# Optimization experiments

Measured on AMD Instinct MI355X. Metric: run time of the kernel, lower is better.

Reference implementation:

```python
import jax, jax.numpy as jnp
import numpy as np

B, HW, D, CL, K, V, NL, H = 16, 4096, 512, 768, 512, 512, 32, 8
EPS = 1e-5

def conv1d(x, w, b):
    # 1x1 Conv1d: x (B, Cin, L), w (Cout, Cin), b (Cout,)
    return jnp.einsum('oi,bil->bol', w, x) + b[:, None]

def inorm(x):
    # InstanceNorm1d (affine=False, biased var) over the length dim per channel
    m = jnp.mean(x, axis=-1, keepdims=True)
    v = jnp.var(x, axis=-1, keepdims=True)
    return (x - m) / jnp.sqrt(v + EPS)

def _forward(x, l, l_mask, w_vis, b_vis, w_langp, b_langp, w_q, b_q, w_k, b_k,
             w_v, b_v, w_lv, b_lv, w_W, b_W, w_langW, b_langW,
             w_mm, b_mm, w_langmm, b_langmm):
    xt = x.transpose(0, 2, 1)                       # (B, D, HW)
    mask = l_mask.transpose(0, 2, 1)                # (B, 1, NL)
    vis = jax.nn.gelu(conv1d(xt, w_vis, b_vis), approximate=False)      # (B, D, HW)
    lang = jax.nn.gelu(conv1d(l, w_langp, b_langp), approximate=False)  # (B, CL, NL)

    q = inorm(conv1d(xt, w_q, b_q)).transpose(0, 2, 1)   # (B, HW, K)
    k = conv1d(l, w_k, b_k) * mask                       # (B, K, NL)
    v = conv1d(l, w_v, b_v) * mask                       # (B, V, NL)
    lv = inorm(conv1d(xt, w_lv, b_lv))                   # (B, CL, HW)

    q = q.reshape(B, HW, H, K // H).transpose(0, 2, 1, 3)   # (B, H, HW, dk)
    k = k.reshape(B, H, K // H, NL)
    v = v.reshape(B, H, V // H, NL)
    lv = lv.reshape(B, H, CL // H, HW)

    # note: scale uses FULL key_channels (as in the torch code), mask bias added once
    sim = jnp.einsum('bhqd,bhdn->bhqn', q, k) * (K ** -0.5)
    sim = sim + (10000.0 * mask[:, :, None, :] - 10000.0)    # (B, H, HW, NL)

    att = jax.nn.softmax(sim, axis=-1)                         # image -> lang
    latt = jax.nn.softmax(sim.transpose(0, 1, 3, 2), axis=-1)  # lang -> image

    lang_out = jnp.einsum('bhnq,bhcq->bhcn', latt, lv).reshape(B, CL, NL) * mask
    lang_out = inorm(conv1d(lang_out, w_langW, b_langW))       # (B, CL, NL)

    out = jnp.einsum('bhqn,bhdn->bqhd', att, v).reshape(B, HW, V)
    vis_out = inorm(conv1d(out.transpose(0, 2, 1), w_W, b_W))  # (B, V, HW)

    mm = jax.nn.gelu(conv1d(vis * vis_out, w_mm, b_mm), approximate=False)
    lang_mm = jax.nn.gelu(conv1d(lang * lang_out, w_langmm, b_langmm), approximate=False)
    return mm.transpose(0, 2, 1), lang_mm.transpose(0, 2, 1)   # (B,HW,V), (B,NL,CL)

def setup_inputs():
    key = jax.random.key(0)
    ks = jax.random.split(key, 24)
    inp = {}
    inp['x'] = jax.random.normal(ks[0], (B, HW, D), jnp.float32)
    inp['l'] = jax.random.normal(ks[1], (B, CL, NL), jnp.float32)
    lengths = jax.random.randint(ks[2], (B, 1), 5, NL + 1)
    inp['l_mask'] = (jnp.arange(NL)[None, :] < lengths).astype(jnp.float32)[:, :, None]
    specs = [('vis', D, D), ('langp', CL, CL), ('q', K, D), ('k', K, CL),
             ('v', V, CL), ('lv', CL, D), ('W', V, V), ('langW', CL, CL),
             ('mm', V, V), ('langmm', CL, CL)]
    for i, (n, o, ci) in enumerate(specs):
        inp['w_' + n] = jax.random.normal(ks[3 + 2 * i], (o, ci), jnp.float32) / float(np.sqrt(ci))
        inp['b_' + n] = jax.random.normal(ks[4 + 2 * i], (o,), jnp.float32) * 0.01
    return inp

def reference(x, l, l_mask, w_vis, b_vis, w_langp, b_langp, w_q, b_q, w_k, b_k,
              w_v, b_v, w_lv, b_lv, w_W, b_W, w_langW, b_langW,
              w_mm, b_mm, w_langmm, b_langmm):
    return _forward(x, l, l_mask, w_vis, b_vis, w_langp, b_langp, w_q, b_q, w_k, b_k,
                    w_v, b_v, w_lv, b_lv, w_W, b_W, w_langW, b_langW,
                    w_mm, b_mm, w_langmm, b_langmm)
```

## Files before the change

kernel.cpp:

```cpp
#include <hip/hip_runtime.h>
#include <cstdint>
#include <cstddef>


typedef __bf16 bf16x8 __attribute__((ext_vector_type(8)));
typedef float f32x4 __attribute__((ext_vector_type(4)));
typedef unsigned short ushort8 __attribute__((ext_vector_type(8)));

__device__ __forceinline__ float bf2f(unsigned short u) {
  union { unsigned int i; float f; } c; c.i = ((unsigned int)u) << 16; return c.f;
}
__device__ __forceinline__ unsigned short f2bf(float f) {
  union { float f; unsigned int i; } c; c.f = f;
  unsigned int r = c.i + 0x7FFFu + ((c.i >> 16) & 1u);
  return (unsigned short)(r >> 16);
}
__device__ __forceinline__ float gelu_f(float x) {
  return 0.5f * x * (1.f + erff(x * 0.70710678118654752f));
}
__device__ __forceinline__ void gload16(const void* g, void* l) {
  __builtin_amdgcn_global_load_lds(
      (__attribute__((address_space(1))) unsigned int*)g,
      (__attribute__((address_space(3))) unsigned int*)l, 16, 0, 0);
}

constexpr size_t OFF_SRQ  = 0;
constexpr size_t OFF_SRLV = OFF_SRQ  + (size_t)16*512*2*4;
constexpr size_t OFF_SRW  = OFF_SRLV + (size_t)16*768*2*4;
constexpr size_t OFF_LACC = OFF_SRW  + (size_t)16*512*2*4;
constexpr size_t SZ_ZERO  = OFF_LACC + (size_t)16*768*32*4;
constexpr size_t OFF_STQ  = SZ_ZERO;
constexpr size_t OFF_STLV = OFF_STQ  + (size_t)16*512*2*4;
constexpr size_t OFF_STW  = OFF_STLV + (size_t)16*768*2*4;
constexpr size_t OFF_KBUF = OFF_STW  + (size_t)16*512*2*4;
constexpr size_t OFF_VBUF = OFF_KBUF + (size_t)16*512*32*4;
constexpr size_t OFF_LANG = OFF_VBUF + (size_t)16*512*32*4;
constexpr size_t OFF_LMX  = OFF_LANG + (size_t)16*768*32*4;
constexpr size_t OFF_LSM  = OFF_LMX  + (size_t)128*32*4;
constexpr size_t OFF_LNORM= OFF_LSM  + (size_t)128*32*4;
constexpr size_t OFF_P2   = OFF_LNORM+ (size_t)16*768*32*4;
constexpr size_t OFF_PMX  = OFF_P2   + (size_t)16*768*32*4;
constexpr size_t OFF_PSM  = OFF_PMX  + (size_t)32*128*32*4;
constexpr size_t OFF_WB   = OFF_PSM  + (size_t)32*128*32*4;
constexpr size_t OFF_Q    = OFF_WB   + (size_t)1441792*2;
constexpr size_t OFF_LV   = OFF_Q    + (size_t)65536*512*2;
constexpr size_t OFF_SIMB = OFF_LV   + (size_t)65536*768*2;

__global__ __launch_bounds__(256) void cvt_bf16(const float* __restrict__ src,
                                                unsigned short* __restrict__ dst, int n8)
{
  int i = blockIdx.x * 256 + threadIdx.x;
  if (i >= n8) return;
  const f32x4* s = (const f32x4*)(src + (size_t)i * 8);
  f32x4 a = s[0], b = s[1];
  ushort8 o;
#pragma unroll
  for (int j = 0; j < 4; ++j) { o[j] = f2bf(a[j]); o[j + 4] = f2bf(b[j]); }
  *(ushort8*)(dst + (size_t)i * 8) = o;
}

template<bool GELU, bool STATS, bool OUTF32>
__global__ __launch_bounds__(256) void gemm_bt(
    const unsigned short* __restrict__ A, const unsigned short* __restrict__ Wb,
    const float* __restrict__ bias, void* __restrict__ Yout,
    float* __restrict__ statsraw, int N, int Kd)
{
  __shared__ __align__(16) unsigned short As[128 * 64];
  __shared__ __align__(16) unsigned short Bs[128 * 64];
  const int t = threadIdx.x;
  const int wave = t >> 6, lane = t & 63;
  const int ln = lane & 15, quad = lane >> 4;
  const int m0 = blockIdx.x * 128, n0 = blockIdx.y * 128;
  const int wm = (wave >> 1) * 64, wn = (wave & 1) * 64;
  const f32x4 fzero = {0.f, 0.f, 0.f, 0.f};
  f32x4 acc[4][4];
#pragma unroll
  for (int i = 0; i < 4; ++i)
#pragma unroll
    for (int j = 0; j < 4; ++j) acc[i][j] = fzero;
  const int lrow = lane >> 3;
  const int lch  = lane & 7;

  for (int k0 = 0; k0 < Kd; k0 += 64) {
#pragma unroll
    for (int it = 0; it < 4; ++it) {
      int g = wave * 4 + it;
      int row = g * 8 + lrow;
      gload16(A  + (size_t)(m0 + row) * Kd + k0 + lch * 8, &As[g * 512]);
      gload16(Wb + (size_t)(n0 + row) * Kd + k0 + lch * 8, &Bs[g * 512]);
    }
    __syncthreads();
#pragma unroll
    for (int kk = 0; kk < 64; kk += 32) {
      int c = (kk >> 3) + quad;
      bf16x8 af[4], bfr[4];
#pragma unroll
      for (int i = 0; i < 4; ++i)
        af[i] = *(const bf16x8*)&As[(wm + i * 16 + ln) * 64 + c * 8];
#pragma unroll
      for (int j = 0; j < 4; ++j)
        bfr[j] = *(const bf16x8*)&Bs[(wn + j * 16 + ln) * 64 + c * 8];
#pragma unroll
      for (int i = 0; i < 4; ++i)
#pragma unroll
        for (int j = 0; j < 4; ++j)
          acc[i][j] = __builtin_amdgcn_mfma_f32_16x16x32_bf16(af[i], bfr[j], acc[i][j], 0, 0, 0);
    }
    __syncthreads();
  }
  float bb[4];
#pragma unroll
  for (int j = 0; j < 4; ++j) bb[j] = bias[n0 + wn + j * 16 + ln];
#pragma unroll
  for (int i = 0; i < 4; ++i)
#pragma unroll
    for (int j = 0; j < 4; ++j)
#pragma unroll
      for (int r = 0; r < 4; ++r) {
        float v = acc[i][j][r] + bb[j];
        if (GELU) v = gelu_f(v);
        acc[i][j][r] = v;
        size_t row = (size_t)(m0 + wm + i * 16 + quad * 4 + r);
        size_t idx = row * N + (n0 + wn + j * 16 + ln);
        if (OUTF32) ((float*)Yout)[idx] = v;
        else ((unsigned short*)Yout)[idx] = f2bf(v);
      }
  if (STATS) {
    float* cs = (float*)As;
    cs[t] = 0.f;
    __syncthreads();
#pragma unroll
    for (int j = 0; j < 4; ++j) {
      float s = 0.f, s2 = 0.f;
#pragma unroll
      for (int i = 0; i < 4; ++i)
#pragma unroll
        for (int r = 0; r < 4; ++r) { float v = acc[i][j][r]; s += v; s2 += v * v; }
      int cl = wn + j * 16 + ln;
      atomicAdd(&cs[cl], s);
      atomicAdd(&cs[128 + cl], s2);
    }
    __syncthreads();
    int bIdx = m0 >> 12;
    if (t < 128) atomicAdd(&statsraw[((size_t)bIdx * N + n0 + t) * 2], cs[t]);
    else atomicAdd(&statsraw[((size_t)bIdx * N + n0 + (t - 128)) * 2 + 1], cs[t]);
  }
}

__global__ void finalize_stats(const float* __restrict__ raw, float* __restrict__ st,
                               int n, float invc) {
  int i = blockIdx.x * 256 + threadIdx.x;
  if (i >= n) return;
  float s = raw[2 * i], s2 = raw[2 * i + 1];
  float m = s * invc;
  float v = fmaxf(s2 * invc - m * m, 0.f);
  st[2 * i] = m;
  st[2 * i + 1] = rsqrtf(v + 1e-5f);
}

template<int EPI>
__global__ __launch_bounds__(256) void sconv(
    const float* __restrict__ l, const float* __restrict__ w,
    const float* __restrict__ bias, const float* __restrict__ lmask,
    float* __restrict__ out, int O, int Cin)
{
  int b = blockIdx.x, og = blockIdx.y;
  int ol = threadIdx.x >> 5, n = threadIdx.x & 31;
  int o = og * 8 + ol;
  const float* lb = l + (size_t)b * Cin * 32 + n;
  const float* wr = w + (size_t)o * Cin;
  float s = 0.f;
#pragma unroll 4
  for (int i = 0; i < Cin; ++i) s += wr[i] * lb[(size_t)i * 32];
  s += bias[o];
  if (EPI == 0) s *= lmask[b * 32 + n];
  else s = gelu_f(s);
  out[((size_t)b * O + o) * 32 + n] = s;
}

__global__ __launch_bounds__(256) void simattv_kernel(
    const unsigned short* __restrict__ qraw, const float* __restrict__ stq,
    const float* __restrict__ kbuf, const float* __restrict__ vbuf,
    const float* __restrict__ lmask,
    unsigned short* __restrict__ simb, unsigned short* __restrict__ outb,
    float* __restrict__ pmx, float* __restrict__ psm)
{
  __shared__ __align__(16) float qs[128][68];
  __shared__ __align__(16) float ks[64][36];
  __shared__ __align__(16) float vs[64][36];
  __shared__ __align__(16) float ss[128][36];
  __shared__ float sm[64], sr[64], mb[32];
  __shared__ float gm[8][32], gs[8][32];
  int qc = blockIdx.x, q0 = qc * 128, h = blockIdx.y, b = blockIdx.z;
  int bh = b * 8 + h;
  int t = threadIdx.x;
  if (t < 64) {
    sm[t] = stq[(b * 512 + h * 64 + t) * 2];
    sr[t] = stq[(b * 512 + h * 64 + t) * 2 + 1];
  } else if (t < 96) {
    mb[t - 64] = 10000.f * (lmask[b * 32 + (t - 64)] - 1.f);
  }
  for (int e = t; e < 2048; e += 256) {
    int d = e >> 5, n = e & 31;
    ks[d][n] = kbuf[((size_t)b * 512 + h * 64 + d) * 32 + n];
    vs[d][n] = vbuf[((size_t)b * 512 + h * 64 + d) * 32 + n];
  }
  __syncthreads();
  const float scale = 0.04419417382415922f;
  for (int e = t; e < 8192; e += 256) {
    int ql = e >> 6, d = e & 63;
    float v = bf2f(qraw[((size_t)(b * 4096) + q0 + ql) * 512 + h * 64 + d]);
    qs[ql][d] = (v - sm[d]) * sr[d] * scale;
  }
  __syncthreads();
  int ql = t >> 1, half = t & 1, nb = half * 16;
  float acc[16];
#pragma unroll
  for (int i = 0; i < 16; ++i) acc[i] = 0.f;
  for (int d = 0; d < 64; ++d) {
    float qv = qs[ql][d];
    const f32x4* kp = (const f32x4*)&ks[d][nb];
#pragma unroll
    for (int u = 0; u < 4; ++u) {
      f32x4 kv = kp[u];
      acc[u * 4 + 0] += qv * kv[0]; acc[u * 4 + 1] += qv * kv[1];
      acc[u * 4 + 2] += qv * kv[2]; acc[u * 4 + 3] += qv * kv[3];
    }
  }
  unsigned short* sg = simb + (((size_t)bh) * 4096 + q0 + ql) * 32 + nb;
#pragma unroll
  for (int i = 0; i < 16; ++i) {
    float v = acc[i] + mb[nb + i];
    ss[ql][nb + i] = v;
    sg[i] = f2bf(v);
  }
  __syncthreads();
  {
    int n2 = t & 31, rg = t >> 5;
    float pm = -1e30f;
#pragma unroll
    for (int r = 0; r < 16; ++r) pm = fmaxf(pm, ss[rg * 16 + r][n2]);
    float psv = 0.f;
#pragma unroll
    for (int r = 0; r < 16; ++r) psv += __expf(ss[rg * 16 + r][n2] - pm);
    gm[rg][n2] = pm; gs[rg][n2] = psv;
  }
  __syncthreads();
  if (t < 32) {
    float M = gm[0][t], S = gs[0][t];
#pragma unroll
    for (int g = 1; g < 8; ++g) {
      float m2 = gm[g][t], s2 = gs[g][t];
      if (m2 > M) { S = S * __expf(M - m2) + s2; M = m2; }
      else S += s2 * __expf(m2 - M);
    }
    pmx[((size_t)qc * 128 + bh) * 32 + t] = M;
    psm[((size_t)qc * 128 + bh) * 32 + t] = S;
  }
  __syncthreads();
  float xv[16];
  float mx = -1e30f;
#pragma unroll
  for (int i = 0; i < 16; ++i) { xv[i] = ss[ql][nb + i]; mx = fmaxf(mx, xv[i]); }
  mx = fmaxf(mx, __shfl_xor(mx, 1));
  float s = 0.f;
#pragma unroll
  for (int i = 0; i < 16; ++i) { xv[i] = __expf(xv[i] - mx); s += xv[i]; }
  s += __shfl_xor(s, 1);
  float inv = 1.f / s;
#pragma unroll
  for (int i = 0; i < 16; ++i) ss[ql][nb + i] = xv[i] * inv;
  __syncthreads();
  float pr[32];
#pragma unroll
  for (int i = 0; i < 8; ++i) ((f32x4*)pr)[i] = ((const f32x4*)&ss[ql][0])[i];
  unsigned short* op = outb + ((size_t)b * 4096 + q0 + ql) * 512 + h * 64 + half * 32;
#pragma unroll
  for (int d = 0; d < 32; ++d) {
    const float* vr = &vs[half * 32 + d][0];
    float a = 0.f;
#pragma unroll
    for (int n4 = 0; n4 < 8; ++n4) {
      f32x4 v4 = *(const f32x4*)&vr[n4 * 4];
      a += pr[n4 * 4 + 0] * v4[0] + pr[n4 * 4 + 1] * v4[1] +
           pr[n4 * 4 + 2] * v4[2] + pr[n4 * 4 + 3] * v4[3];
    }
    op[d] = f2bf(a);
  }
}

__global__ __launch_bounds__(256) void latt_merge(const float* __restrict__ pmx,
                                                  const float* __restrict__ psm,
                                                  float* __restrict__ lmx,
                                                  float* __restrict__ lsm)
{
  int i = blockIdx.x * 256 + threadIdx.x;
  int bh = i >> 5, n = i & 31;
  float M = -1e30f, S = 0.f;
#pragma unroll 4
  for (int c = 0; c < 32; ++c) {
    float m2 = pmx[((size_t)c * 128 + bh) * 32 + n];
    float s2 = psm[((size_t)c * 128 + bh) * 32 + n];
    if (m2 > M) { S = S * __expf(M - m2) + s2; M = m2; }
    else S += s2 * __expf(m2 - M);
  }
  lmx[bh * 32 + n] = M;
  lsm[bh * 32 + n] = S;
}

__global__ __launch_bounds__(256) void langout_acc_kernel(
    const unsigned short* __restrict__ simb, const float* __restrict__ lmx,
    const float* __restrict__ lsm, const unsigned short* __restrict__ lvraw,
    const float* __restrict__ stlv, float* __restrict__ lacc)
{
  __shared__ __align__(16) float pt[64][32];
  __shared__ __align__(16) float lvt[64][96];
  __shared__ float cm[96], cr[96], lm[32], li[32];
  int bh = blockIdx.x, b = bh >> 3, h = bh & 7;
  int qs0 = blockIdx.y * 512;
  int t = threadIdx.x;
  if (t < 96) { cm[t] = stlv[(b * 768 + h * 96 + t) * 2]; cr[t] = stlv[(b * 768 + h * 96 + t) * 2 + 1]; }
  else if (t >= 128 && t < 160) {
    int n = t - 128;
    lm[n] = lmx[bh * 32 + n];
    li[n] = 1.f / lsm[bh * 32 + n];
  }
  __syncthreads();
  int n = t & 31, cg = t >> 5;
  float acc[12];
#pragma unroll
  for (int r = 0; r < 12; ++r) acc[r] = 0.f;
  for (int c0 = 0; c0 < 512; c0 += 64) {
    if (c0) __syncthreads();
#pragma unroll
    for (int i = 0; i < 8; ++i) {
      int e = t + 256 * i;
      int ql = e >> 5, nn = e & 31;
      float x = bf2f(simb[((size_t)bh * 4096 + qs0 + c0 + ql) * 32 + nn]);
      pt[ql][nn] = __expf(x - lm[nn]) * li[nn];
    }
#pragma unroll
    for (int i = 0; i < 24; ++i) {
      int e = t + 256 * i;
      int ql = e / 96, cc = e % 96;
      float v = bf2f(lvraw[((size_t)(b * 4096) + qs0 + c0 + ql) * 768 + h * 96 + cc]);
      lvt[ql][cc] = (v - cm[cc]) * cr[cc];
    }
    __syncthreads();
    for (int q = 0; q < 64; ++q) {
      float pv = pt[q][n];
      const f32x4* lp = (const f32x4*)&lvt[q][cg * 12];
      f32x4 a0 = lp[0], a1 = lp[1], a2 = lp[2];
      acc[0] += pv * a0[0]; acc[1] += pv * a0[1]; acc[2]  += pv * a0[2]; acc[3]  += pv * a0[3];
      acc[4] += pv * a1[0]; acc[5] += pv * a1[1]; acc[6]  += pv * a1[2]; acc[7]  += pv * a1[3];
      acc[8] += pv * a2[0]; acc[9] += pv * a2[1]; acc[10] += pv * a2[2]; acc[11] += pv * a2[3];
    }
  }
#pragma unroll
  for (int r = 0; r < 12; ++r)
    atomicAdd(&lacc[((size_t)b * 768 + h * 96 + cg * 12 + r) * 32 + n], acc[r]);
}

__global__ __launch_bounds__(256) void prod_kernel(
    const unsigned short* __restrict__ visb, const unsigned short* __restrict__ wraw,
    const float* __restrict__ stw, unsigned short* __restrict__ P)
{
  size_t idx = ((size_t)blockIdx.x * 256 + threadIdx.x) * 8;
  int b = (int)(idx >> 21);
  int c = (int)(idx & 511);
  ushort8 vv = *(const ushort8*)&visb[idx];
  ushort8 wv = *(const ushort8*)&wraw[idx];
  ushort8 pv;
#pragma unroll
  for (int i = 0; i < 8; ++i) {
    float mean = stw[(b * 512 + c + i) * 2], rs = stw[(b * 512 + c + i) * 2 + 1];
    pv[i] = f2bf(bf2f(vv[i]) * ((bf2f(wv[i]) - mean) * rs));
  }
  *(ushort8*)&P[idx] = pv;
}

__global__ __launch_bounds__(256) void langW_kernel(
    const float* __restrict__ lacc, const float* __restrict__ w,
    const float* __restrict__ bias, const float* __restrict__ lmask,
    float* __restrict__ lnorm)
{
  int b = blockIdx.x, og = blockIdx.y;
  int ol = threadIdx.x >> 5, n = threadIdx.x & 31;
  int o = og * 8 + ol;
  const float* ab = lacc + (size_t)b * 768 * 32 + n;
  const float* wr = w + (size_t)o * 768;
  float s = 0.f;
#pragma unroll 4
  for (int i = 0; i < 768; ++i) s += wr[i] * ab[(size_t)i * 32];
  float y = s * lmask[b * 32 + n] + bias[o];
  float m = y;
#pragma unroll
  for (int off = 16; off >= 1; off >>= 1) m += __shfl_xor(m, off);
  m *= (1.f / 32.f);
  float d = y - m;
  float vv = d * d;
#pragma unroll
  for (int off = 16; off >= 1; off >>= 1) vv += __shfl_xor(vv, off);
  vv *= (1.f / 32.f);
  lnorm[((size_t)b * 768 + o) * 32 + n] = d * rsqrtf(vv + 1e-5f);
}

__global__ __launch_bounds__(256) void p2_kernel(const float* __restrict__ a,
                                                 const float* __restrict__ b,
                                                 float* __restrict__ o, int n) {
  int i = blockIdx.x * 256 + threadIdx.x;
  if (i < n) o[i] = a[i] * b[i];
}

__global__ __launch_bounds__(256) void langmm_kernel(
    const float* __restrict__ p2, const float* __restrict__ w,
    const float* __restrict__ bias, float* __restrict__ out1)
{
  int b = blockIdx.x, og = blockIdx.y;
  int ol = threadIdx.x >> 5, n = threadIdx.x & 31;
  int o = og * 8 + ol;
  const float* pb = p2 + (size_t)b * 768 * 32 + n;
  const float* wr = w + (size_t)o * 768;
  float s = 0.f;
#pragma unroll 4
  for (int i = 0; i < 768; ++i) s += wr[i] * pb[(size_t)i * 32];
  s = gelu_f(s + bias[o]);
  __shared__ float tile[8][32];
  tile[ol][n] = s;
  __syncthreads();
  int nn = threadIdx.x >> 3, cl = threadIdx.x & 7;
  out1[((size_t)b * 32 + nn) * 768 + og * 8 + cl] = tile[cl][nn];
}

extern "C" void kernel_launch(void* const* d_in, const int* in_sizes, int n_in,
                              void* d_out, int out_size, void* d_ws, size_t ws_size,
                              hipStream_t stream)
{
  (void)in_sizes; (void)n_in; (void)out_size; (void)ws_size;
  const float* x       = (const float*)d_in[0];
  const float* l       = (const float*)d_in[1];
  const float* lmask   = (const float*)d_in[2];
  const float* w_vis   = (const float*)d_in[3];
  const float* b_vis   = (const float*)d_in[4];
  const float* w_langp = (const float*)d_in[5];
  const float* b_langp = (const float*)d_in[6];
  const float* w_q     = (const float*)d_in[7];
  const float* b_q     = (const float*)d_in[8];
  const float* w_k     = (const float*)d_in[9];
  const float* b_k     = (const float*)d_in[10];
  const float* w_v     = (const float*)d_in[11];
  const float* b_v     = (const float*)d_in[12];
  const float* w_lv    = (const float*)d_in[13];
  const float* b_lv    = (const float*)d_in[14];
  const float* w_W     = (const float*)d_in[15];
  const float* b_W     = (const float*)d_in[16];
  const float* w_langW = (const float*)d_in[17];
  const float* b_langW = (const float*)d_in[18];
  const float* w_mm    = (const float*)d_in[19];
  const float* b_mm    = (const float*)d_in[20];
  const float* w_langmm= (const float*)d_in[21];
  const float* b_langmm= (const float*)d_in[22];

  char* ws = (char*)d_ws;
  float* srq  = (float*)(ws + OFF_SRQ);
  float* srlv = (float*)(ws + OFF_SRLV);
  float* srw  = (float*)(ws + OFF_SRW);
  float* lacc = (float*)(ws + OFF_LACC);
  float* stq  = (float*)(ws + OFF_STQ);
  float* stlv = (float*)(ws + OFF_STLV);
  float* stw  = (float*)(ws + OFF_STW);
  float* kbuf = (float*)(ws + OFF_KBUF);
  float* vbuf = (float*)(ws + OFF_VBUF);
  float* lang = (float*)(ws + OFF_LANG);
  float* lmx  = (float*)(ws + OFF_LMX);
  float* lsm  = (float*)(ws + OFF_LSM);
  float* lnorm= (float*)(ws + OFF_LNORM);
  float* p2   = (float*)(ws + OFF_P2);
  float* pmx  = (float*)(ws + OFF_PMX);
  float* psm  = (float*)(ws + OFF_PSM);
  unsigned short* wb    = (unsigned short*)(ws + OFF_WB);
  unsigned short* wbvis = wb;
  unsigned short* wbq   = wb + 262144;
  unsigned short* wblv  = wb + 524288;
  unsigned short* wbW   = wb + 917504;
  unsigned short* wbmm  = wb + 1179648;
  unsigned short* qraw  = (unsigned short*)(ws + OFF_Q);
  unsigned short* lvraw = (unsigned short*)(ws + OFF_LV);
  unsigned short* wraw  = (unsigned short*)(ws + OFF_LV);
  unsigned short* simb  = (unsigned short*)(ws + OFF_SIMB);
  float* out0 = (float*)d_out;
  float* out1 = out0 + (size_t)16 * 4096 * 512;
  unsigned short* visb = (unsigned short*)d_out;
  unsigned short* xb   = (unsigned short*)d_out + 33554432;

  hipMemsetAsync(ws, 0, SZ_ZERO, stream);

  cvt_bf16<<<16384, 256, 0, stream>>>(x, xb, 4194304);
  cvt_bf16<<<128, 256, 0, stream>>>(w_vis, wbvis, 32768);
  cvt_bf16<<<128, 256, 0, stream>>>(w_q,   wbq,   32768);
  cvt_bf16<<<192, 256, 0, stream>>>(w_lv,  wblv,  49152);
  cvt_bf16<<<128, 256, 0, stream>>>(w_W,   wbW,   32768);
  cvt_bf16<<<128, 256, 0, stream>>>(w_mm,  wbmm,  32768);

  sconv<1><<<dim3(16, 96), 256, 0, stream>>>(l, w_langp, b_langp, lmask, lang, 768, 768);
  sconv<0><<<dim3(16, 64), 256, 0, stream>>>(l, w_k, b_k, lmask, kbuf, 512, 768);
  sconv<0><<<dim3(16, 64), 256, 0, stream>>>(l, w_v, b_v, lmask, vbuf, 512, 768);

  gemm_bt<true,  false, false><<<dim3(512, 4), 256, 0, stream>>>(xb, wbvis, b_vis, visb, nullptr, 512, 512);
  gemm_bt<false, true,  false><<<dim3(512, 4), 256, 0, stream>>>(xb, wbq,   b_q,   qraw,  srq,   512, 512);
  gemm_bt<false, true,  false><<<dim3(512, 6), 256, 0, stream>>>(xb, wblv,  b_lv,  lvraw, srlv,  768, 512);
  finalize_stats<<<32, 256, 0, stream>>>(srq,  stq,  16 * 512, 1.f / 4096.f);
  finalize_stats<<<48, 256, 0, stream>>>(srlv, stlv, 16 * 768, 1.f / 4096.f);

  simattv_kernel<<<dim3(32, 8, 16), 256, 0, stream>>>(qraw, stq, kbuf, vbuf, lmask, simb, qraw, pmx, psm);
  latt_merge<<<16, 256, 0, stream>>>(pmx, psm, lmx, lsm);
  langout_acc_kernel<<<dim3(128, 8), 256, 0, stream>>>(simb, lmx, lsm, lvraw, stlv, lacc);

  gemm_bt<false, true,  false><<<dim3(512, 4), 256, 0, stream>>>(qraw, wbW, b_W, wraw, srw, 512, 512);
  finalize_stats<<<32, 256, 0, stream>>>(srw, stw, 16 * 512, 1.f / 4096.f);
  prod_kernel<<<16384, 256, 0, stream>>>(visb, wraw, stw, qraw);
  gemm_bt<true,  false, true ><<<dim3(512, 4), 256, 0, stream>>>(qraw, wbmm, b_mm, out0, nullptr, 512, 512);

  langW_kernel<<<dim3(16, 96), 256, 0, stream>>>(lacc, w_langW, b_langW, lmask, lnorm);
  p2_kernel<<<1536, 256, 0, stream>>>(lang, lnorm, p2, 16 * 768 * 32);
  langmm_kernel<<<dim3(16, 96), 256, 0, stream>>>(p2, w_langmm, b_langmm, out1);
}
```

Measured before the change: 1.375 ms.

## Move sim and att·V in simattv kernel to bf16 MFMA with split-precision operands

Rewrites the attention kernel so the q·k similarity and the softmax·V product run on 16x16x32 bf16 MFMA instructions instead of scalar FP32 FMAs. K and V are stored in LDS as hi/lo bf16 pairs to keep near-FP32 accuracy. The instance-norm mean of q is folded into a per-column bias and the scale into K, so q is fed raw from global memory. Row and column softmax statistics are now computed with cross-lane shuffles on the MFMA accumulators, which removes the fp32 LDS staging buffers and several barriers. The cost is extra MFMAs for the lo parts and reduced precision on q and P.

```diff
diff --git a/kernel.cpp b/kernel.cpp
--- a/kernel.cpp
+++ b/kernel.cpp
@@ -6,6 +6,7 @@
 typedef __bf16 bf16x8 __attribute__((ext_vector_type(8)));
 typedef float f32x4 __attribute__((ext_vector_type(4)));
 typedef unsigned short ushort8 __attribute__((ext_vector_type(8)));
+typedef unsigned short us4 __attribute__((ext_vector_type(4)));
 
 __device__ __forceinline__ float bf2f(unsigned short u) {
   union { unsigned int i; float f; } c; c.i = ((unsigned int)u) << 16; return c.f;
@@ -185,107 +186,165 @@
     unsigned short* __restrict__ simb, unsigned short* __restrict__ outb,
     float* __restrict__ pmx, float* __restrict__ psm)
 {
-  __shared__ __align__(16) float qs[128][68];
-  __shared__ __align__(16) float ks[64][36];
-  __shared__ __align__(16) float vs[64][36];
-  __shared__ __align__(16) float ss[128][36];
-  __shared__ float sm[64], sr[64], mb[32];
-  __shared__ float gm[8][32], gs[8][32];
-  int qc = blockIdx.x, q0 = qc * 128, h = blockIdx.y, b = blockIdx.z;
-  int bh = b * 8 + h;
-  int t = threadIdx.x;
+  __shared__ __align__(16) unsigned short kThi[32][72];
+  __shared__ __align__(16) unsigned short kTlo[32][72];
+  __shared__ __align__(16) unsigned short vshi[64][40];
+  __shared__ __align__(16) unsigned short vslo[64][40];
+  __shared__ __align__(16) unsigned short pq[4][32][40];
+  __shared__ float sm[64], srs[64], cb[32];
+  __shared__ float wmax[4][32], wsum[4][32];
+
+  const int qc = blockIdx.x, q0 = qc * 128, h = blockIdx.y, b = blockIdx.z;
+  const int bh = b * 8 + h;
+  const int t = threadIdx.x;
+  const int wv = t >> 6, lane = t & 63, ln = lane & 15, quad = lane >> 4;
+  const float scale = 0.04419417382415922f;
+
   if (t < 64) {
-    sm[t] = stq[(b * 512 + h * 64 + t) * 2];
-    sr[t] = stq[(b * 512 + h * 64 + t) * 2 + 1];
-  } else if (t < 96) {
-    mb[t - 64] = 10000.f * (lmask[b * 32 + (t - 64)] - 1.f);
-  }
+    sm[t]  = stq[(b * 512 + h * 64 + t) * 2];
+    srs[t] = stq[(b * 512 + h * 64 + t) * 2 + 1] * scale;
+  }
+  __syncthreads();
+
+  const float* kb = kbuf + ((size_t)b * 512 + h * 64) * 32;
+  const float* vb = vbuf + ((size_t)b * 512 + h * 64) * 32;
   for (int e = t; e < 2048; e += 256) {
     int d = e >> 5, n = e & 31;
-    ks[d][n] = kbuf[((size_t)b * 512 + h * 64 + d) * 32 + n];
-    vs[d][n] = vbuf[((size_t)b * 512 + h * 64 + d) * 32 + n];
-  }
+    float kv = kb[e] * srs[d];
+    unsigned short khi = f2bf(kv);
+    kThi[n][d] = khi;
+    kTlo[n][d] = f2bf(kv - bf2f(khi));
+    float vv = vb[e];
+    unsigned short vhi = f2bf(vv);
+    vshi[d][n] = vhi;
+    vslo[d][n] = f2bf(vv - bf2f(vhi));
+  }
+  if (t < 32) {
+    float s = 0.f;
+#pragma unroll 8
+    for (int d = 0; d < 64; ++d) s += sm[d] * srs[d] * kb[d * 32 + t];
+    cb[t] = 10000.f * (lmask[b * 32 + t] - 1.f) - s;
+  }
+
+  const unsigned short* qbase = qraw + ((size_t)(b * 4096) + q0 + wv * 32) * 512 + h * 64;
+  bf16x8 qfr[2][2];
+#pragma unroll
+  for (int qf = 0; qf < 2; ++qf)
+#pragma unroll
+    for (int kf = 0; kf < 2; ++kf)
+      qfr[qf][kf] = *(const bf16x8*)(qbase + (size_t)(qf * 16 + ln) * 512 + kf * 32 + quad * 8);
   __syncthreads();
-  const float scale = 0.04419417382415922f;
-  for (int e = t; e < 8192; e += 256) {
-    int ql = e >> 6, d = e & 63;
-    float v = bf2f(qraw[((size_t)(b * 4096) + q0 + ql) * 512 + h * 64 + d]);
-    qs[ql][d] = (v - sm[d]) * sr[d] * scale;
+
+  const f32x4 fz = {0.f, 0.f, 0.f, 0.f};
+  f32x4 accS[2][2] = {{fz, fz}, {fz, fz}};
+#pragma unroll
+  for (int kf = 0; kf < 2; ++kf) {
+#pragma unroll
+    for (int nf = 0; nf < 2; ++nf) {
+      bf16x8 kh = *(const bf16x8*)&kThi[nf * 16 + ln][kf * 32 + quad * 8];
+      bf16x8 kl = *(const bf16x8*)&kTlo[nf * 16 + ln][kf * 32 + quad * 8];
+#pragma unroll
+      for (int qf = 0; qf < 2; ++qf) {
+        accS[qf][nf] = __builtin_amdgcn_mfma_f32_16x16x32_bf16(qfr[qf][kf], kh, accS[qf][nf], 0, 0, 0);
+        accS[qf][nf] = __builtin_amdgcn_mfma_f32_16x16x32_bf16(qfr[qf][kf], kl, accS[qf][nf], 0, 0, 0);
+      }
+    }
+  }
+  float cb0 = cb[ln], cb1 = cb[16 + ln];
+#pragma unroll
+  for (int qf = 0; qf < 2; ++qf)
+#pragma unroll
+    for (int r = 0; r < 4; ++r) {
+      accS[qf][0][r] += cb0;
+      accS[qf][1][r] += cb1;
+    }
+  {
+    unsigned short* sgb = simb + ((size_t)bh * 4096 + q0 + wv * 32) * 32;
+#pragma unroll
+    for (int qf = 0; qf < 2; ++qf)
+#pragma unroll
+      for (int r = 0; r < 4; ++r) {
+        size_t rowo = (size_t)(qf * 16 + quad * 4 + r) * 32;
+        sgb[rowo + ln]      = f2bf(accS[qf][0][r]);
+        sgb[rowo + 16 + ln] = f2bf(accS[qf][1][r]);
+      }
+  }
+#pragma unroll
+  for (int nf = 0; nf < 2; ++nf) {
+    float m = accS[0][nf][0];
+#pragma unroll
+    for (int r = 1; r < 4; ++r) m = fmaxf(m, accS[0][nf][r]);
+#pragma unroll
+    for (int r = 0; r < 4; ++r) m = fmaxf(m, accS[1][nf][r]);
+    m = fmaxf(m, __shfl_xor(m, 16));
+    m = fmaxf(m, __shfl_xor(m, 32));
+    float s = 0.f;
+#pragma unroll
+    for (int qf = 0; qf < 2; ++qf)
+#pragma unroll
+      for (int r = 0; r < 4; ++r) s += __expf(accS[qf][nf][r] - m);
+    s += __shfl_xor(s, 16);
+    s += __shfl_xor(s, 32);
+    if (quad == 0) { wmax[wv][nf * 16 + ln] = m; wsum[wv][nf * 16 + ln] = s; }
+  }
+#pragma unroll
+  for (int qf = 0; qf < 2; ++qf) {
+#pragma unroll
+    for (int r = 0; r < 4; ++r) {
+      float a0 = accS[qf][0][r], a1 = accS[qf][1][r];
+      float m = fmaxf(a0, a1);
+      m = fmaxf(m, __shfl_xor(m, 1));
+      m = fmaxf(m, __shfl_xor(m, 2));
+      m = fmaxf(m, __shfl_xor(m, 4));
+      m = fmaxf(m, __shfl_xor(m, 8));
+      float e0 = __expf(a0 - m), e1 = __expf(a1 - m);
+      float s = e0 + e1;
+      s += __shfl_xor(s, 1);
+      s += __shfl_xor(s, 2);
+      s += __shfl_xor(s, 4);
+      s += __shfl_xor(s, 8);
+      float inv = 1.f / s;
+      int row = qf * 16 + quad * 4 + r;
+      pq[wv][row][ln]      = f2bf(e0 * inv);
+      pq[wv][row][16 + ln] = f2bf(e1 * inv);
+    }
   }
   __syncthreads();
-  int ql = t >> 1, half = t & 1, nb = half * 16;
-  float acc[16];
-#pragma unroll
-  for (int i = 0; i < 16; ++i) acc[i] = 0.f;
-  for (int d = 0; d < 64; ++d) {
-    float qv = qs[ql][d];
-    const f32x4* kp = (const f32x4*)&ks[d][nb];
-#pragma unroll
-    for (int u = 0; u < 4; ++u) {
-      f32x4 kv = kp[u];
-      acc[u * 4 + 0] += qv * kv[0]; acc[u * 4 + 1] += qv * kv[1];
-      acc[u * 4 + 2] += qv * kv[2]; acc[u * 4 + 3] += qv * kv[3];
-    }
-  }
-  unsigned short* sg = simb + (((size_t)bh) * 4096 + q0 + ql) * 32 + nb;
-#pragma unroll
-  for (int i = 0; i < 16; ++i) {
-    float v = acc[i] + mb[nb + i];
-    ss[ql][nb + i] = v;
-    sg[i] = f2bf(v);
-  }
-  __syncthreads();
-  {
-    int n2 = t & 31, rg = t >> 5;
-    float pm = -1e30f;
-#pragma unroll
-    for (int r = 0; r < 16; ++r) pm = fmaxf(pm, ss[rg * 16 + r][n2]);
-    float psv = 0.f;
-#pragma unroll
-    for (int r = 0; r < 16; ++r) psv += __expf(ss[rg * 16 + r][n2] - pm);
-    gm[rg][n2] = pm; gs[rg][n2] = psv;
+  bf16x8 vfh[4], vfl[4];
+#pragma unroll
+  for (int mf = 0; mf < 4; ++mf) {
+    vfh[mf] = *(const bf16x8*)&vshi[mf * 16 + ln][quad * 8];
+    vfl[mf] = *(const bf16x8*)&vslo[mf * 16 + ln][quad * 8];
+  }
+#pragma unroll
+  for (int nf = 0; nf < 2; ++nf) {
+    bf16x8 pb = *(const bf16x8*)&pq[wv][nf * 16 + ln][quad * 8];
+    f32x4 accO[4] = {fz, fz, fz, fz};
+#pragma unroll
+    for (int mf = 0; mf < 4; ++mf) {
+      accO[mf] = __builtin_amdgcn_mfma_f32_16x16x32_bf16(vfh[mf], pb, accO[mf], 0, 0, 0);
+      accO[mf] = __builtin_amdgcn_mfma_f32_16x16x32_bf16(vfl[mf], pb, accO[mf], 0, 0, 0);
+    }
+    unsigned short* op = outb + ((size_t)(b * 4096) + q0 + wv * 32 + nf * 16 + ln) * 512 + h * 64;
+#pragma unroll
+    for (int mf = 0; mf < 4; ++mf) {
+      us4 o;
+#pragma unroll
+      for (int r = 0; r < 4; ++r) o[r] = f2bf(accO[mf][r]);
+      *(us4*)(op + mf * 16 + quad * 4) = o;
+    }
   }
   __syncthreads();
   if (t < 32) {
-    float M = gm[0][t], S = gs[0][t];
-#pragma unroll
-    for (int g = 1; g < 8; ++g) {
-      float m2 = gm[g][t], s2 = gs[g][t];
+    float M = wmax[0][t], S = wsum[0][t];
+#pragma unroll
+    for (int g = 1; g < 4; ++g) {
+      float m2 = wmax[g][t], s2 = wsum[g][t];
       if (m2 > M) { S = S * __expf(M - m2) + s2; M = m2; }
       else S += s2 * __expf(m2 - M);
     }
     pmx[((size_t)qc * 128 + bh) * 32 + t] = M;
     psm[((size_t)qc * 128 + bh) * 32 + t] = S;
-  }
-  __syncthreads();
-  float xv[16];
-  float mx = -1e30f;
-#pragma unroll
-  for (int i = 0; i < 16; ++i) { xv[i] = ss[ql][nb + i]; mx = fmaxf(mx, xv[i]); }
-  mx = fmaxf(mx, __shfl_xor(mx, 1));
-  float s = 0.f;
-#pragma unroll
-  for (int i = 0; i < 16; ++i) { xv[i] = __expf(xv[i] - mx); s += xv[i]; }
-  s += __shfl_xor(s, 1);
-  float inv = 1.f / s;
-#pragma unroll
-  for (int i = 0; i < 16; ++i) ss[ql][nb + i] = xv[i] * inv;
-  __syncthreads();
-  float pr[32];
-#pragma unroll
-  for (int i = 0; i < 8; ++i) ((f32x4*)pr)[i] = ((const f32x4*)&ss[ql][0])[i];
-  unsigned short* op = outb + ((size_t)b * 4096 + q0 + ql) * 512 + h * 64 + half * 32;
-#pragma unroll
-  for (int d = 0; d < 32; ++d) {
-    const float* vr = &vs[half * 32 + d][0];
-    float a = 0.f;
-#pragma unroll
-    for (int n4 = 0; n4 < 8; ++n4) {
-      f32x4 v4 = *(const f32x4*)&vr[n4 * 4];
-      a += pr[n4 * 4 + 0] * v4[0] + pr[n4 * 4 + 1] * v4[1] +
-           pr[n4 * 4 + 2] * v4[2] + pr[n4 * 4 + 3] * v4[3];
-    }
-    op[d] = f2bf(a);
   }
 }
 
```

Measured after the change: 1.305 ms. -5.1%, faster.
